# Performance work log

Measured on AMD Instinct MI355X. Metric: run time of the kernel, lower is better.

## Reference

```python
import jax, jax.numpy as jnp
import numpy as np

BIG = 1e10  # large finite value standing in for +inf in masked mins (grad-safe)


def setup_inputs() -> dict:
    key = jax.random.key(0)
    k1, k2, k3 = jax.random.split(key, 3)
    B, C, N = 16, 3, 4096
    x = jax.random.normal(k1, (B, C, N), dtype=jnp.float32)
    y = jax.random.normal(k2, (B, C, N), dtype=jnp.float32)
    mask = jax.random.randint(k3, (B, N), 0, 2, dtype=jnp.int32)
    return {"x": x, "y": y, "mask": mask}


def reference(x, y, mask):
    # x, y: (B, 3, N); mask: (B, N) with 1 = valid point
    xt = jnp.swapaxes(x, 1, 2)  # (B, N, 3)
    yt = jnp.swapaxes(y, 1, 2)  # (B, N, 3)
    xx = jnp.sum(xt * xt, axis=-1)  # (B, N)
    yy = jnp.sum(yt * yt, axis=-1)  # (B, N)
    # squared pairwise distances, P[b, n, m] = ||x_bn - y_bm||^2
    P = xx[:, :, None] + yy[:, None, :] - 2.0 * jnp.einsum("bnd,bmd->bnm", xt, yt)

    valid = mask.astype(bool)                 # (B, N)
    mf = mask.astype(P.dtype)                 # (B, N)
    cnt = jnp.sum(mf, axis=1)                 # (B,) number of valid points per batch

    # direction 1: for each y-point m, min over valid x-rows n; mean over valid m
    mins1 = jnp.min(jnp.where(valid[:, :, None], P, BIG), axis=1)  # (B, N)
    means1 = jnp.sum(mins1 * mf, axis=1) / cnt                      # (B,)

    # direction 2: for each x-point m, min over valid y-cols n; mean over valid m
    mins2 = jnp.min(jnp.where(valid[:, None, :], P, BIG), axis=2)  # (B, N)
    means2 = jnp.sum(mins2 * mf, axis=1) / cnt                      # (B,)

    return jnp.mean(means1) + jnp.mean(means2)
```

## Files before the change

kernel.cpp:

```cpp
#include <hip/hip_runtime.h>

typedef short bf16x8 __attribute__((ext_vector_type(8)));
typedef float f32x4  __attribute__((ext_vector_type(4)));

#define BIG_F 1e10f
constexpr int B = 16;
constexpr int N = 4096;
constexpr int ROWS = 256;
constexpr int COLS = 512;
constexpr int NRB = N / ROWS;
constexpr int NCB = N / COLS;

__device__ __forceinline__ void split(float v, unsigned short& h, unsigned short& l) {
    unsigned hb = __float_as_uint(v) & 0xFFFF0000u;
    h = (unsigned short)(hb >> 16);
    float r = v - __uint_as_float(hb);
    l = (unsigned short)(__float_as_uint(r) >> 16);
}

__device__ __forceinline__ float min3f(float a, float b, float c) {
    return fminf(fminf(a, b), c);
}

__global__ __launch_bounds__(256) void chamfer_mfma(
    const float* __restrict__ x, const float* __restrict__ y,
    const int* __restrict__ mask,
    float* __restrict__ rowpart,
    float* __restrict__ colpart,
    float* __restrict__ out)
{
    const int rb = blockIdx.x & 15;
    const int cb = blockIdx.x >> 4;
    const int b  = blockIdx.y;
    const int t  = threadIdx.x;

    __shared__ unsigned short Apack[ROWS * 16];
    __shared__ unsigned short Bpack[COLS * 16];
    __shared__ float colbuf[4][COLS];

    if (blockIdx.x == 0 && b == 0 && t == 0) out[0] = 0.0f;

    const unsigned short one = 0x3F80;

    {
        int n = rb * ROWS + t;
        const float* xb = x + (size_t)b * 3 * N;
        float x0 = xb[n], x1 = xb[N + n], x2 = xb[2 * N + n];
        float madd = mask[b * N + n] ? 0.0f : BIG_F;
        float xx = fmaf(x2, x2, fmaf(x1, x1, x0 * x0)) + madd;
        unsigned short ah0, al0, ah1, al1, ah2, al2, xh, xl;
        split(-2.0f * x0, ah0, al0);
        split(-2.0f * x1, ah1, al1);
        split(-2.0f * x2, ah2, al2);
        split(xx, xh, xl);
        unsigned short* p = &Apack[t * 16];
        p[0] = ah0; p[1] = ah1; p[2] = ah2; p[3] = ah0; p[4] = ah1; p[5] = ah2;
        p[6] = al0; p[7] = al1; p[8] = al2; p[9] = al0; p[10] = al1; p[11] = al2;
        p[12] = xh; p[13] = xl; p[14] = one; p[15] = one;
    }
#pragma unroll
    for (int i = 0; i < 2; ++i) {
        int c = t + i * 256;
        int m = cb * COLS + c;
        const float* yb = y + (size_t)b * 3 * N;
        float y0 = yb[m], y1 = yb[N + m], y2 = yb[2 * N + m];
        float madd = mask[b * N + m] ? 0.0f : BIG_F;
        float yy = fmaf(y2, y2, fmaf(y1, y1, y0 * y0)) + madd;
        unsigned short yh0, yl0, yh1, yl1, yh2, yl2, qh, ql;
        split(y0, yh0, yl0);
        split(y1, yh1, yl1);
        split(y2, yh2, yl2);
        split(yy, qh, ql);
        unsigned short* p = &Bpack[c * 16];
        p[0] = yh0; p[1] = yh1; p[2] = yh2; p[3] = yl0; p[4] = yl1; p[5] = yl2;
        p[6] = yh0; p[7] = yh1; p[8] = yh2; p[9] = yl0; p[10] = yl1; p[11] = yl2;
        p[12] = one; p[13] = one; p[14] = qh; p[15] = ql;
    }
    __syncthreads();

    const int w  = t >> 6;
    const int L  = t & 63;
    const int lq = L >> 4;
    const int lc = L & 15;

    const bf16x8 zero8 = {0, 0, 0, 0, 0, 0, 0, 0};
    const f32x4  zf4   = {0.f, 0.f, 0.f, 0.f};

    bf16x8 afr[4];
#pragma unroll
    for (int s = 0; s < 4; ++s) {
        afr[s] = zero8;
        if (lq < 2)
            afr[s] = *(const bf16x8*)&Apack[(w * 64 + s * 16 + lc) * 16 + lq * 8];
    }

    float rm[4][4];
#pragma unroll
    for (int s = 0; s < 4; ++s)
#pragma unroll
        for (int r = 0; r < 4; ++r) rm[s][r] = 1e30f;

    for (int cc = 0; cc < 16; ++cc) {
        const int c0 = cc * 32 + lc;
        bf16x8 bf0 = zero8, bf1 = zero8;
        if (lq < 2) {
            bf0 = *(const bf16x8*)&Bpack[c0 * 16 + lq * 8];
            bf1 = *(const bf16x8*)&Bpack[(c0 + 16) * 16 + lq * 8];
        }
        f32x4 C0[4], C1[4];
#pragma unroll
        for (int s = 0; s < 4; ++s) {
            C0[s] = __builtin_amdgcn_mfma_f32_16x16x32_bf16(afr[s], bf0, zf4, 0, 0, 0);
            C1[s] = __builtin_amdgcn_mfma_f32_16x16x32_bf16(afr[s], bf1, zf4, 0, 0, 0);
        }
        float v0 = 1e30f, v1 = 1e30f;
#pragma unroll
        for (int s = 0; s < 4; ++s)
#pragma unroll
            for (int r = 0; r < 4; ++r) {
                rm[s][r] = min3f(rm[s][r], C0[s][r], C1[s][r]);
                v0 = fminf(v0, C0[s][r]);
                v1 = fminf(v1, C1[s][r]);
            }
        v0 = fminf(v0, __shfl_xor(v0, 16));
        v0 = fminf(v0, __shfl_xor(v0, 32));
        v1 = fminf(v1, __shfl_xor(v1, 16));
        v1 = fminf(v1, __shfl_xor(v1, 32));
        if (lq == 0) {
            colbuf[w][cc * 32 + lc] = v0;
            colbuf[w][cc * 32 + 16 + lc] = v1;
        }
    }

#pragma unroll
    for (int off = 1; off <= 8; off <<= 1)
#pragma unroll
        for (int s = 0; s < 4; ++s)
#pragma unroll
            for (int r = 0; r < 4; ++r)
                rm[s][r] = fminf(rm[s][r], __shfl_xor(rm[s][r], off));
    if (lc == 0) {
        float* rp = rowpart + ((size_t)b * NCB + cb) * N + rb * ROWS + w * 64;
#pragma unroll
        for (int s = 0; s < 4; ++s)
#pragma unroll
            for (int r = 0; r < 4; ++r)
                rp[s * 16 + lq * 4 + r] = rm[s][r];
    }

    __syncthreads();
    for (int c = t; c < COLS; c += 256) {
        float v = fminf(fminf(colbuf[0][c], colbuf[1][c]),
                        fminf(colbuf[2][c], colbuf[3][c]));
        colpart[((size_t)b * NRB + rb) * N + cb * COLS + c] = v;
    }
}

__global__ __launch_bounds__(256) void finalize_kernel(
    const int* __restrict__ mask,
    const float* __restrict__ rowpart, const float* __restrict__ colpart,
    float* __restrict__ out)
{
    const int b   = blockIdx.x & 15;
    const int dir = (blockIdx.x >> 4) & 1;
    const int q   = blockIdx.x >> 5;
    const int t   = threadIdx.x;
    const int* mrow = mask + b * N;

    int cnt = 0;
    for (int i = t; i < N / 4; i += 256) {
        int4 mk = ((const int4*)mrow)[i];
        cnt += mk.x + mk.y + mk.z + mk.w;
    }

    const float* base = dir ? (colpart + (size_t)b * NRB * N)
                            : (rowpart + (size_t)b * NCB * N);
    const int npb = dir ? NRB : NCB;

    const int p0 = q * 1024 + t * 4;
    float4 mn = *(const float4*)(base + p0);
    for (int pb = 1; pb < npb; ++pb) {
        float4 v = *(const float4*)(base + (size_t)pb * N + p0);
        mn.x = fminf(mn.x, v.x); mn.y = fminf(mn.y, v.y);
        mn.z = fminf(mn.z, v.z); mn.w = fminf(mn.w, v.w);
    }
    int4 mk = *(const int4*)(mrow + p0);
    float s = (mk.x ? mn.x : 0.f) + (mk.y ? mn.y : 0.f)
            + (mk.z ? mn.z : 0.f) + (mk.w ? mn.w : 0.f);

    for (int off = 32; off > 0; off >>= 1) {
        s   += __shfl_down(s, off);
        cnt += __shfl_down(cnt, off);
    }
    __shared__ float rs[4];
    __shared__ int   rc[4];
    const int wv = t >> 6;
    if ((t & 63) == 0) { rs[wv] = s; rc[wv] = cnt; }
    __syncthreads();
    if (t == 0) {
        float S = rs[0] + rs[1] + rs[2] + rs[3];
        float C = (float)(rc[0] + rc[1] + rc[2] + rc[3]);
        atomicAdd(out, (S / C) * (1.0f / 16.0f));
    }
}

extern "C" void kernel_launch(void* const* d_in, const int* in_sizes, int n_in,
                              void* d_out, int out_size, void* d_ws, size_t ws_size,
                              hipStream_t stream) {
    const float* x    = (const float*)d_in[0];
    const float* y    = (const float*)d_in[1];
    const int*   mask = (const int*)d_in[2];

    float* rowpart = (float*)d_ws;
    float* colpart = rowpart + (size_t)B * NCB * N;

    chamfer_mfma<<<dim3(NRB * NCB, B), 256, 0, stream>>>(
        x, y, mask, rowpart, colpart, (float*)d_out);
    finalize_kernel<<<dim3(128), 256, 0, stream>>>(
        mask, rowpart, colpart, (float*)d_out);
}
```

Measured before the change: 96.04 us.

## Switch to 32x32x16 bf16 MFMA with padded LDS and prefetched B fragments

Replaces the 16x16x32 MFMA tiling, where half the lanes carried zero K-fragments, with 32x32x16 MFMAs whose K=16 exactly matches the packed operand width, so no lanes are wasted. This cuts the MFMA count per tile and the cross-lane shuffles needed for the column minimum. The LDS row stride is padded from 16 to 20 shorts to reduce bank conflicts, and the next B fragment is prefetched one iteration ahead. In exchange, the row-min reduction now needs an extra shuffle stage and the accumulators use more registers per lane.

After: 106.9 us. 1.11x slower.

```diff
diff --git a/kernel.cpp b/kernel.cpp
--- a/kernel.cpp
+++ b/kernel.cpp
@@ -1,7 +1,7 @@
 #include <hip/hip_runtime.h>
 
 typedef short bf16x8 __attribute__((ext_vector_type(8)));
-typedef float f32x4  __attribute__((ext_vector_type(4)));
+typedef float f32x16 __attribute__((ext_vector_type(16)));
 
 #define BIG_F 1e10f
 constexpr int B = 16;
@@ -10,6 +10,8 @@
 constexpr int COLS = 512;
 constexpr int NRB = N / ROWS;
 constexpr int NCB = N / COLS;
+constexpr int NCC = COLS / 32;
+constexpr int PST = 20;
 
 __device__ __forceinline__ void split(float v, unsigned short& h, unsigned short& l) {
     unsigned hb = __float_as_uint(v) & 0xFFFF0000u;
@@ -34,8 +36,8 @@
     const int b  = blockIdx.y;
     const int t  = threadIdx.x;
 
-    __shared__ unsigned short Apack[ROWS * 16];
-    __shared__ unsigned short Bpack[COLS * 16];
+    __shared__ unsigned short Apack[ROWS * PST];
+    __shared__ unsigned short Bpack[COLS * PST];
     __shared__ float colbuf[4][COLS];
 
     if (blockIdx.x == 0 && b == 0 && t == 0) out[0] = 0.0f;
@@ -53,7 +55,7 @@
         split(-2.0f * x1, ah1, al1);
         split(-2.0f * x2, ah2, al2);
         split(xx, xh, xl);
-        unsigned short* p = &Apack[t * 16];
+        unsigned short* p = &Apack[t * PST];
         p[0] = ah0; p[1] = ah1; p[2] = ah2; p[3] = ah0; p[4] = ah1; p[5] = ah2;
         p[6] = al0; p[7] = al1; p[8] = al2; p[9] = al0; p[10] = al1; p[11] = al2;
         p[12] = xh; p[13] = xl; p[14] = one; p[15] = one;
@@ -71,7 +73,7 @@
         split(y1, yh1, yl1);
         split(y2, yh2, yl2);
         split(yy, qh, ql);
-        unsigned short* p = &Bpack[c * 16];
+        unsigned short* p = &Bpack[c * PST];
         p[0] = yh0; p[1] = yh1; p[2] = yh2; p[3] = yl0; p[4] = yl1; p[5] = yl2;
         p[6] = yh0; p[7] = yh1; p[8] = yh2; p[9] = yl0; p[10] = yl1; p[11] = yl2;
         p[12] = one; p[13] = one; p[14] = qh; p[15] = ql;
@@ -80,72 +82,67 @@
 
     const int w  = t >> 6;
     const int L  = t & 63;
-    const int lq = L >> 4;
-    const int lc = L & 15;
-
-    const bf16x8 zero8 = {0, 0, 0, 0, 0, 0, 0, 0};
-    const f32x4  zf4   = {0.f, 0.f, 0.f, 0.f};
-
-    bf16x8 afr[4];
-#pragma unroll
-    for (int s = 0; s < 4; ++s) {
-        afr[s] = zero8;
-        if (lq < 2)
-            afr[s] = *(const bf16x8*)&Apack[(w * 64 + s * 16 + lc) * 16 + lq * 8];
-    }
-
-    float rm[4][4];
-#pragma unroll
-    for (int s = 0; s < 4; ++s)
-#pragma unroll
-        for (int r = 0; r < 4; ++r) rm[s][r] = 1e30f;
-
-    for (int cc = 0; cc < 16; ++cc) {
-        const int c0 = cc * 32 + lc;
-        bf16x8 bf0 = zero8, bf1 = zero8;
-        if (lq < 2) {
-            bf0 = *(const bf16x8*)&Bpack[c0 * 16 + lq * 8];
-            bf1 = *(const bf16x8*)&Bpack[(c0 + 16) * 16 + lq * 8];
+    const int h  = L >> 5;
+    const int ln = L & 31;
+
+    bf16x8 afr[2];
+#pragma unroll
+    for (int s = 0; s < 2; ++s)
+        afr[s] = *(const bf16x8*)&Apack[(w * 64 + s * 32 + ln) * PST + h * 8];
+
+    float rm[2][16];
+#pragma unroll
+    for (int s = 0; s < 2; ++s)
+#pragma unroll
+        for (int i = 0; i < 16; ++i) rm[s][i] = 1e30f;
+
+    bf16x8 nbf = *(const bf16x8*)&Bpack[ln * PST + h * 8];
+
+    for (int cc = 0; cc < NCC; ++cc) {
+        bf16x8 bf = nbf;
+        if (cc + 1 < NCC)
+            nbf = *(const bf16x8*)&Bpack[((cc + 1) * 32 + ln) * PST + h * 8];
+
+        f32x16 C0, C1;
+        {
+            f32x16 z = {};
+            C0 = __builtin_amdgcn_mfma_f32_32x32x16_bf16(afr[0], bf, z, 0, 0, 0);
+            C1 = __builtin_amdgcn_mfma_f32_32x32x16_bf16(afr[1], bf, z, 0, 0, 0);
         }
-        f32x4 C0[4], C1[4];
-#pragma unroll
-        for (int s = 0; s < 4; ++s) {
-            C0[s] = __builtin_amdgcn_mfma_f32_16x16x32_bf16(afr[s], bf0, zf4, 0, 0, 0);
-            C1[s] = __builtin_amdgcn_mfma_f32_16x16x32_bf16(afr[s], bf1, zf4, 0, 0, 0);
+#pragma unroll
+        for (int i = 0; i < 16; ++i) {
+            rm[0][i] = fminf(rm[0][i], C0[i]);
+            rm[1][i] = fminf(rm[1][i], C1[i]);
         }
-        float v0 = 1e30f, v1 = 1e30f;
-#pragma unroll
-        for (int s = 0; s < 4; ++s)
-#pragma unroll
-            for (int r = 0; r < 4; ++r) {
-                rm[s][r] = min3f(rm[s][r], C0[s][r], C1[s][r]);
-                v0 = fminf(v0, C0[s][r]);
-                v1 = fminf(v1, C1[s][r]);
-            }
-        v0 = fminf(v0, __shfl_xor(v0, 16));
-        v0 = fminf(v0, __shfl_xor(v0, 32));
-        v1 = fminf(v1, __shfl_xor(v1, 16));
-        v1 = fminf(v1, __shfl_xor(v1, 32));
-        if (lq == 0) {
-            colbuf[w][cc * 32 + lc] = v0;
-            colbuf[w][cc * 32 + 16 + lc] = v1;
-        }
-    }
-
-#pragma unroll
-    for (int off = 1; off <= 8; off <<= 1)
-#pragma unroll
-        for (int s = 0; s < 4; ++s)
-#pragma unroll
-            for (int r = 0; r < 4; ++r)
-                rm[s][r] = fminf(rm[s][r], __shfl_xor(rm[s][r], off));
-    if (lc == 0) {
+        float v = fminf(fminf(min3f(C0[0], C0[1], C0[2]),
+                              min3f(C0[3], C0[4], C0[5])),
+                        fminf(min3f(C0[6], C0[7], C0[8]),
+                              min3f(C0[9], C0[10], C0[11])));
+        v = fminf(v, fminf(fminf(C0[12], C0[13]), fminf(C0[14], C0[15])));
+        float v1 = fminf(fminf(min3f(C1[0], C1[1], C1[2]),
+                               min3f(C1[3], C1[4], C1[5])),
+                         fminf(min3f(C1[6], C1[7], C1[8]),
+                               min3f(C1[9], C1[10], C1[11])));
+        v1 = fminf(v1, fminf(fminf(C1[12], C1[13]), fminf(C1[14], C1[15])));
+        v = fminf(v, v1);
+        v = fminf(v, __shfl_xor(v, 32));
+        if (h == 0) colbuf[w][cc * 32 + ln] = v;
+    }
+
+#pragma unroll
+    for (int off = 1; off <= 16; off <<= 1)
+#pragma unroll
+        for (int s = 0; s < 2; ++s)
+#pragma unroll
+            for (int i = 0; i < 16; ++i)
+                rm[s][i] = fminf(rm[s][i], __shfl_xor(rm[s][i], off));
+    if (ln == 0) {
         float* rp = rowpart + ((size_t)b * NCB + cb) * N + rb * ROWS + w * 64;
 #pragma unroll
-        for (int s = 0; s < 4; ++s)
-#pragma unroll
-            for (int r = 0; r < 4; ++r)
-                rp[s * 16 + lq * 4 + r] = rm[s][r];
+        for (int s = 0; s < 2; ++s)
+#pragma unroll
+            for (int i = 0; i < 16; ++i)
+                rp[s * 32 + (i & 3) + 8 * (i >> 2) + 4 * h] = rm[s][i];
     }
 
     __syncthreads();
```
